# Kernel tuning notes

Measured on AMD Instinct MI355X. Metric: run time of the kernel, lower is better.

Reference implementation:

```python
import jax, jax.numpy as jnp
import numpy as np

T, B, F, H, P = 256, 512, 256, 512, 12  # seq len, batch, feature_dim, hidden_dim, p_interval


def setup_inputs() -> dict:
    key = jax.random.key(0)
    ks = jax.random.split(key, 9)
    s = 1.0 / np.sqrt(F + H)  # torch Linear default init scale
    def lin(k):
        kw, kb = jax.random.split(k)
        W = jax.random.uniform(kw, (F + H, H), jnp.float32, -s, s)
        b = jax.random.uniform(kb, (H,), jnp.float32, -s, s)
        return W, b
    Wf, bf = lin(ks[0])
    Wi, bi = lin(ks[1])
    Wo, bo = lin(ks[2])
    Wg, bg = lin(ks[3])
    x = jax.random.normal(ks[4], (T, B, F), jnp.float32)
    return {"x": x, "Wf": Wf, "bf": bf, "Wi": Wi, "bi": bi,
            "Wo": Wo, "bo": bo, "Wg": Wg, "bg": bg}


def _slstm(x, Wf, bf, Wi, bi, Wo, bo, Wg, bg):
    Tn, Bn, _ = x.shape
    h0 = jnp.zeros((P, Bn, H), x.dtype)
    # NOTE: original torch code reassigns c to a 2D [B,H] tensor after step 0,
    # so c[t % P] indexes a batch ROW (shape [H]) that broadcasts. At t=0 the
    # slice is all-zeros either way, so carrying a 2D c is exactly faithful.
    c0 = jnp.zeros((Bn, H), x.dtype)

    def step(carry, inp):
        h, c = carry
        x_t, t = inp
        idx = t % P
        xc = jnp.concatenate([x_t, h[idx]], axis=1)  # [B, F+H]
        f = jax.nn.softmax(xc @ Wf + bf, axis=1)
        i = jax.nn.softmax(xc @ Wi + bi, axis=1)
        o = jax.nn.softmax(xc @ Wo + bo, axis=1)
        g = jnp.tanh(xc @ Wg + bg)
        c_new = jnp.tanh(f * c[idx] + i * g)  # c[idx]: row [H], broadcasts over B
        h = h.at[idx].set(o * c_new)
        return (h, c_new), None

    (h, _), _ = jax.lax.scan(step, (h0, c0), (x, jnp.arange(Tn)))
    return h[(Tn - 1) % P]


def reference(x, Wf, bf, Wi, bi, Wo, bo, Wg, bg):
    return _slstm(x, Wf, bf, Wi, bi, Wo, bo, Wg, bg)
```

## Files before the change

### kernel.cpp

```cpp
#include <hip/hip_runtime.h>

typedef unsigned short u16;
typedef unsigned int   u32;

typedef __attribute__((ext_vector_type(8))) short bf16x8;
typedef __attribute__((ext_vector_type(16))) float f32x16;

__device__ __forceinline__ u16 f2bf(float v) {
    u32 u = __float_as_uint(v);
    u32 r = (u + 0x7fffu + ((u >> 16) & 1u)) >> 16;
    return (u16)r;
}
__device__ __forceinline__ float bf2f(u16 h) { return __uint_as_float(((u32)h) << 16); }

__device__ __forceinline__ float ftanh(float x) {
    float e = __expf(2.0f * x);
    return 1.0f - 2.0f * __builtin_amdgcn_rcpf(e + 1.0f);
}

__device__ __forceinline__ void gl2lds16(const void* g, void* l) {
    __builtin_amdgcn_global_load_lds(
        (const __attribute__((address_space(1))) void*)g,
        (__attribute__((address_space(3))) void*)l, 16, 0, 0);
}

__global__ void init_k(u16* __restrict__ hh, u16* __restrict__ hl, float* __restrict__ cb) {
    int i = blockIdx.x * 256 + threadIdx.x;
    hh[i] = 0; hl[i] = 0;
    if (i < 2 * 512) cb[i] = 0.0f;
}

__global__ void pack_w(const float* __restrict__ Wf, const float* __restrict__ bf_,
                       const float* __restrict__ Wi, const float* __restrict__ bi_,
                       const float* __restrict__ Wo, const float* __restrict__ bo_,
                       const float* __restrict__ Wg, const float* __restrict__ bg_,
                       u16* __restrict__ wth, u16* __restrict__ wtl, float* __restrict__ bias4) {
    int idx = blockIdx.x * 256 + threadIdx.x;
    int n = idx / 768, k = idx - n * 768;
    int gate = n >> 9, col = n & 511;
    const float* W = (gate == 0) ? Wf : (gate == 1) ? Wi : (gate == 2) ? Wo : Wg;
    float v = W[k * 512 + col];
    u16 h = f2bf(v);
    wth[idx] = h;
    wtl[idx] = f2bf(v - bf2f(h));
    if (k == 0) {
        const float* bb = (gate == 0) ? bf_ : (gate == 1) ? bi_ : (gate == 2) ? bo_ : bg_;
        bias4[n] = bb[col];
    }
}

__global__ void split_x(const float* __restrict__ src, u16* __restrict__ oh, u16* __restrict__ ol) {
    int i = blockIdx.x * 256 + threadIdx.x;
    float4 v = ((const float4*)src)[i];
    u16 hx = f2bf(v.x), hy = f2bf(v.y), hz = f2bf(v.z), hw = f2bf(v.w);
    u16 lx = f2bf(v.x - bf2f(hx)), ly = f2bf(v.y - bf2f(hy));
    u16 lz = f2bf(v.z - bf2f(hz)), lw = f2bf(v.w - bf2f(hw));
    uint2 hv; hv.x = (u32)hx | ((u32)hy << 16); hv.y = (u32)hz | ((u32)hw << 16);
    uint2 lv; lv.x = (u32)lx | ((u32)ly << 16); lv.y = (u32)lz | ((u32)lw << 16);
    ((uint2*)oh)[i] = hv;
    ((uint2*)ol)[i] = lv;
}

#define BK 32
__global__ __launch_bounds__(256, 3) void gemm_x3(
    const u16* __restrict__ xh, const u16* __restrict__ xl,
    const u16* __restrict__ hh, const u16* __restrict__ hl,
    const u16* __restrict__ wth, const u16* __restrict__ wtl,
    const float* __restrict__ bias4, float* __restrict__ lg) {
    __shared__ __align__(16) u16 Ah[128 * BK];
    __shared__ __align__(16) u16 Al[128 * BK];
    __shared__ __align__(16) u16 Bh[128 * BK];
    __shared__ __align__(16) u16 Bl[128 * BK];

    const int tid = threadIdx.x;
    const int wid = tid >> 6, lane = tid & 63;
    const int bm = blockIdx.x, bn = blockIdx.y;
    const int s = bm >> 2;
    const int b0 = (bm & 3) * 128;
    const int laneR = lane >> 2;
    const int laneC = (lane & 3) * 8;

    u16* lds = (wid == 0) ? Ah : (wid == 1) ? Al : (wid == 2) ? Bh : Bl;
    const u16* xp = (wid == 0) ? xh : xl;
    const u16* hp = (wid == 0) ? hh : hl;
    const u16* wp = (wid == 2) ? wth : wtl;
    const u16* xrow = xp + (size_t)(s * 512 + b0) * 256 + laneR * 256 + laneC;
    const u16* hrow = hp + (size_t)(s * 512 + b0) * 512 + laneR * 512 + laneC;
    const u16* wrow = wp + (size_t)(bn * 128) * 768 + laneR * 768 + laneC;

    const int wm = wid >> 1, wn = wid & 1;
    const int l32 = lane & 31, khalf = lane >> 5;

    f32x16 acc[2][2];
#pragma unroll
    for (int i = 0; i < 2; i++)
#pragma unroll
        for (int j = 0; j < 2; j++)
#pragma unroll
            for (int r = 0; r < 16; ++r) acc[i][j][r] = 0.f;

    for (int k0 = 0; k0 < 768; k0 += BK) {
        __syncthreads();
        if (wid < 2) {
            if (k0 < 256) {
                const u16* src = xrow + k0;
#pragma unroll
                for (int r = 0; r < 8; ++r) gl2lds16(src + r * 16 * 256, lds + r * 16 * BK);
            } else {
                const u16* src = hrow + (k0 - 256);
#pragma unroll
                for (int r = 0; r < 8; ++r) gl2lds16(src + r * 16 * 512, lds + r * 16 * BK);
            }
        } else {
            const u16* src = wrow + k0;
#pragma unroll
            for (int r = 0; r < 8; ++r) gl2lds16(src + r * 16 * 768, lds + r * 16 * BK);
        }
        __syncthreads();

        bf16x8 a_h[2][2], a_l[2][2], b_h[2][2], b_l[2][2];
#pragma unroll
        for (int t = 0; t < 2; ++t)
#pragma unroll
            for (int ks = 0; ks < 2; ++ks) {
                int ko = ks * 16 + khalf * 8;
                a_h[t][ks] = *(const bf16x8*)&Ah[(wm * 64 + t * 32 + l32) * BK + ko];
                a_l[t][ks] = *(const bf16x8*)&Al[(wm * 64 + t * 32 + l32) * BK + ko];
                b_h[t][ks] = *(const bf16x8*)&Bh[(wn * 64 + t * 32 + l32) * BK + ko];
                b_l[t][ks] = *(const bf16x8*)&Bl[(wn * 64 + t * 32 + l32) * BK + ko];
            }
#pragma unroll
        for (int ks = 0; ks < 2; ++ks)
#pragma unroll
            for (int i = 0; i < 2; ++i)
#pragma unroll
                for (int j = 0; j < 2; ++j) {
                    acc[i][j] = __builtin_amdgcn_mfma_f32_32x32x16_bf16(a_h[i][ks], b_h[j][ks], acc[i][j], 0, 0, 0);
                    acc[i][j] = __builtin_amdgcn_mfma_f32_32x32x16_bf16(a_h[i][ks], b_l[j][ks], acc[i][j], 0, 0, 0);
                    acc[i][j] = __builtin_amdgcn_mfma_f32_32x32x16_bf16(a_l[i][ks], b_h[j][ks], acc[i][j], 0, 0, 0);
                }
    }

#pragma unroll
    for (int j = 0; j < 2; ++j) {
        int n = bn * 128 + wn * 64 + j * 32 + l32;
        float bv = bias4[n];
#pragma unroll
        for (int i = 0; i < 2; ++i) {
            int rbase = wm * 64 + i * 32 + 4 * khalf;
#pragma unroll
            for (int r = 0; r < 16; ++r) {
                int row = rbase + (r & 3) + 8 * (r >> 2);
                __builtin_nontemporal_store(acc[i][j][r] + bv,
                    &lg[(size_t)(bm * 128 + row) * 2048 + n]);
            }
        }
    }
}

__device__ __forceinline__ void chain_step(const float* __restrict__ lg, int j, int lane, float r[8]) {
    int rowb = (j + 1) % 12;
    const float* base = lg + (size_t)(j * 512 + rowb) * 2048 + lane * 8;
    float f[8], iv[8], g[8];
#pragma unroll
    for (int u = 0; u < 8; ++u) { f[u] = base[u]; iv[u] = base[512 + u]; g[u] = base[1536 + u]; }
    float mf = -1e30f, mi = -1e30f;
#pragma unroll
    for (int u = 0; u < 8; ++u) { mf = fmaxf(mf, f[u]); mi = fmaxf(mi, iv[u]); }
#pragma unroll
    for (int o = 32; o; o >>= 1) { mf = fmaxf(mf, __shfl_xor(mf, o)); mi = fmaxf(mi, __shfl_xor(mi, o)); }
    float sf = 0.f, si = 0.f;
#pragma unroll
    for (int u = 0; u < 8; ++u) {
        f[u] = __expf(f[u] - mf); sf += f[u];
        iv[u] = __expf(iv[u] - mi); si += iv[u];
    }
#pragma unroll
    for (int o = 32; o; o >>= 1) { sf += __shfl_xor(sf, o); si += __shfl_xor(si, o); }
    float rf = __builtin_amdgcn_rcpf(sf), ri = __builtin_amdgcn_rcpf(si);
#pragma unroll
    for (int u = 0; u < 8; ++u) {
        float gg = ftanh(g[u]);
        r[u] = ftanh(f[u] * rf * r[u] + iv[u] * ri * gg);
    }
}

__global__ __launch_bounds__(256) void gates_k(
    const float* __restrict__ lg, float* __restrict__ cb,
    u16* __restrict__ hh, u16* __restrict__ hl,
    float* __restrict__ out, int t0, int S, int rd, int wr) {
    __shared__ float rsh[512];
    const int widx = threadIdx.x >> 6, lane = threadIdx.x & 63;
    const int s = (S - 1) - (blockIdx.x >> 7);
    const int b = (blockIdx.x & 127) * 4 + widx;
    const int t = t0 + s;

    if (widx == 0) {
        float r[8];
#pragma unroll
        for (int u = 0; u < 8; ++u) r[u] = cb[rd * 512 + lane * 8 + u];
        for (int j = 0; j < s; ++j) chain_step(lg, j, lane, r);
#pragma unroll
        for (int u = 0; u < 8; ++u) rsh[lane * 8 + u] = r[u];
        if ((int)blockIdx.x == 127 && t0 + S < 256) {
            chain_step(lg, S - 1, lane, r);
#pragma unroll
            for (int u = 0; u < 8; ++u) cb[wr * 512 + lane * 8 + u] = r[u];
        }
    }
    __syncthreads();

    const float* row = lg + (size_t)(s * 512 + b) * 2048 + lane * 8;
    float f[8], iv[8], ov[8], g[8];
#pragma unroll
    for (int u = 0; u < 8; ++u) {
        f[u] = row[u]; iv[u] = row[512 + u]; ov[u] = row[1024 + u]; g[u] = row[1536 + u];
    }
    float mf = -1e30f, mi = -1e30f, mo = -1e30f;
#pragma unroll
    for (int u = 0; u < 8; ++u) { mf = fmaxf(mf, f[u]); mi = fmaxf(mi, iv[u]); mo = fmaxf(mo, ov[u]); }
#pragma unroll
    for (int o = 32; o; o >>= 1) {
        mf = fmaxf(mf, __shfl_xor(mf, o));
        mi = fmaxf(mi, __shfl_xor(mi, o));
        mo = fmaxf(mo, __shfl_xor(mo, o));
    }
    float sf = 0.f, si = 0.f, so = 0.f;
#pragma unroll
    for (int u = 0; u < 8; ++u) {
        f[u] = __expf(f[u] - mf); sf += f[u];
        iv[u] = __expf(iv[u] - mi); si += iv[u];
        ov[u] = __expf(ov[u] - mo); so += ov[u];
    }
#pragma unroll
    for (int o = 32; o; o >>= 1) {
        sf += __shfl_xor(sf, o); si += __shfl_xor(si, o); so += __shfl_xor(so, o);
    }
    float rf = __builtin_amdgcn_rcpf(sf), ri = __builtin_amdgcn_rcpf(si), ro = __builtin_amdgcn_rcpf(so);
    float hout[8];
#pragma unroll
    for (int u = 0; u < 8; ++u) {
        float rr = rsh[lane * 8 + u];
        float gg = ftanh(g[u]);
        float cv = ftanh(f[u] * rf * rr + iv[u] * ri * gg);
        hout[u] = ov[u] * ro * cv;
    }
    u32 hhp[4], hlp[4];
#pragma unroll
    for (int u = 0; u < 4; ++u) {
        u16 h0 = f2bf(hout[2 * u]), h1 = f2bf(hout[2 * u + 1]);
        u16 l0 = f2bf(hout[2 * u] - bf2f(h0)), l1 = f2bf(hout[2 * u + 1] - bf2f(h1));
        hhp[u] = (u32)h0 | ((u32)h1 << 16);
        hlp[u] = (u32)l0 | ((u32)l1 << 16);
    }
    size_t hb = ((size_t)(s * 512 + b)) * 512 + lane * 8;
    *(uint4*)&hh[hb] = make_uint4(hhp[0], hhp[1], hhp[2], hhp[3]);
    *(uint4*)&hl[hb] = make_uint4(hlp[0], hlp[1], hlp[2], hlp[3]);
    if (t == 255) {
        float* op = out + (size_t)b * 512 + lane * 8;
#pragma unroll
        for (int u = 0; u < 8; ++u) op[u] = hout[u];
    }
}

extern "C" void kernel_launch(void* const* d_in, const int* in_sizes, int n_in,
                              void* d_out, int out_size, void* d_ws, size_t ws_size,
                              hipStream_t stream) {
    const float* x   = (const float*)d_in[0];
    const float* Wf  = (const float*)d_in[1];
    const float* bf_ = (const float*)d_in[2];
    const float* Wi  = (const float*)d_in[3];
    const float* bi_ = (const float*)d_in[4];
    const float* Wo  = (const float*)d_in[5];
    const float* bo_ = (const float*)d_in[6];
    const float* Wg  = (const float*)d_in[7];
    const float* bg_ = (const float*)d_in[8];
    float* out = (float*)d_out;

    char* p = (char*)d_ws;
    u16* xh  = (u16*)p; p += 134217728;
    u16* xl  = (u16*)p; p += 134217728;
    u16* wth = (u16*)p; p += 3145728;
    u16* wtl = (u16*)p; p += 3145728;
    u16* hh  = (u16*)p; p += 6291456;
    u16* hl  = (u16*)p; p += 6291456;
    float* bias4 = (float*)p; p += 8192;
    float* cb    = (float*)p; p += 4096;
    float* lg    = (float*)p; p += 50331648;

    init_k<<<12288, 256, 0, stream>>>(hh, hl, cb);
    pack_w<<<6144, 256, 0, stream>>>(Wf, bf_, Wi, bi_, Wo, bo_, Wg, bg_, wth, wtl, bias4);
    split_x<<<32768, 256, 0, stream>>>(x, xh, xl);

    for (int blk = 0; blk < 22; ++blk) {
        int t0 = blk * 12;
        int S = (256 - t0 >= 12) ? 12 : (256 - t0);
        gemm_x3<<<dim3(S * 4, 16), 256, 0, stream>>>(
            xh + (size_t)t0 * 512 * 256, xl + (size_t)t0 * 512 * 256,
            hh, hl, wth, wtl, bias4, lg);
        gates_k<<<S * 128, 256, 0, stream>>>(lg, cb, hh, hl, out, t0, S, blk & 1, (blk + 1) & 1);
    }
}
```

Baseline: 1.975 ms.

## Double-buffer activation tiles in LDS and stream weights directly from global

The activation (A) tiles in the split-bf16 GEMM now use a two-stage LDS buffer. The next K-slice is prefetched with global-to-LDS loads while the current one is consumed, so each iteration needs one barrier instead of two. The weight (B) tiles no longer go through LDS: each wave reads its bf16 high and low fragments straight from global memory into registers. This cuts LDS traffic and synchronization, but exposes global-load latency for the weights and makes both waves sharing a column slice fetch the same weight data redundantly.

```diff
diff --git a/kernel.cpp b/kernel.cpp
--- a/kernel.cpp
+++ b/kernel.cpp
@@ -67,10 +67,7 @@
     const u16* __restrict__ hh, const u16* __restrict__ hl,
     const u16* __restrict__ wth, const u16* __restrict__ wtl,
     const float* __restrict__ bias4, float* __restrict__ lg) {
-    __shared__ __align__(16) u16 Ah[128 * BK];
-    __shared__ __align__(16) u16 Al[128 * BK];
-    __shared__ __align__(16) u16 Bh[128 * BK];
-    __shared__ __align__(16) u16 Bl[128 * BK];
+    __shared__ __align__(16) u16 Abuf[2][2][128 * BK];
 
     const int tid = threadIdx.x;
     const int wid = tid >> 6, lane = tid & 63;
@@ -80,17 +77,18 @@
     const int laneR = lane >> 2;
     const int laneC = (lane & 3) * 8;
 
-    u16* lds = (wid == 0) ? Ah : (wid == 1) ? Al : (wid == 2) ? Bh : Bl;
     const u16* xp = (wid == 0) ? xh : xl;
     const u16* hp = (wid == 0) ? hh : hl;
-    const u16* wp = (wid == 2) ? wth : wtl;
     const u16* xrow = xp + (size_t)(s * 512 + b0) * 256 + laneR * 256 + laneC;
     const u16* hrow = hp + (size_t)(s * 512 + b0) * 512 + laneR * 512 + laneC;
-    const u16* wrow = wp + (size_t)(bn * 128) * 768 + laneR * 768 + laneC;
 
     const int wm = wid >> 1, wn = wid & 1;
     const int l32 = lane & 31, khalf = lane >> 5;
 
+    const size_t brow = (size_t)(bn * 128 + wn * 64 + l32) * 768 + khalf * 8;
+    const u16* bhp = wth + brow;
+    const u16* blp = wtl + brow;
+
     f32x16 acc[2][2];
 #pragma unroll
     for (int i = 0; i < 2; i++)
@@ -98,36 +96,49 @@
         for (int j = 0; j < 2; j++)
 #pragma unroll
             for (int r = 0; r < 16; ++r) acc[i][j][r] = 0.f;
+
+    if (wid < 2) {
+        u16* dst = Abuf[0][wid];
+#pragma unroll
+        for (int r = 0; r < 8; ++r) gl2lds16(xrow + r * 16 * 256, dst + r * 16 * BK);
+    }
 
     for (int k0 = 0; k0 < 768; k0 += BK) {
         __syncthreads();
-        if (wid < 2) {
-            if (k0 < 256) {
-                const u16* src = xrow + k0;
-#pragma unroll
-                for (int r = 0; r < 8; ++r) gl2lds16(src + r * 16 * 256, lds + r * 16 * BK);
+        const int cur = (k0 / BK) & 1;
+        if (wid < 2 && k0 + BK < 768) {
+            u16* dst = Abuf[cur ^ 1][wid];
+            int k1 = k0 + BK;
+            if (k1 < 256) {
+                const u16* src = xrow + k1;
+#pragma unroll
+                for (int r = 0; r < 8; ++r) gl2lds16(src + r * 16 * 256, dst + r * 16 * BK);
             } else {
-                const u16* src = hrow + (k0 - 256);
-#pragma unroll
-                for (int r = 0; r < 8; ++r) gl2lds16(src + r * 16 * 512, lds + r * 16 * BK);
+                const u16* src = hrow + (k1 - 256);
+#pragma unroll
+                for (int r = 0; r < 8; ++r) gl2lds16(src + r * 16 * 512, dst + r * 16 * BK);
             }
-        } else {
-            const u16* src = wrow + k0;
-#pragma unroll
-            for (int r = 0; r < 8; ++r) gl2lds16(src + r * 16 * 768, lds + r * 16 * BK);
         }
-        __syncthreads();
-
-        bf16x8 a_h[2][2], a_l[2][2], b_h[2][2], b_l[2][2];
+
+        bf16x8 b_h[2][2], b_l[2][2];
 #pragma unroll
         for (int t = 0; t < 2; ++t)
 #pragma unroll
             for (int ks = 0; ks < 2; ++ks) {
-                int ko = ks * 16 + khalf * 8;
-                a_h[t][ks] = *(const bf16x8*)&Ah[(wm * 64 + t * 32 + l32) * BK + ko];
-                a_l[t][ks] = *(const bf16x8*)&Al[(wm * 64 + t * 32 + l32) * BK + ko];
-                b_h[t][ks] = *(const bf16x8*)&Bh[(wn * 64 + t * 32 + l32) * BK + ko];
-                b_l[t][ks] = *(const bf16x8*)&Bl[(wn * 64 + t * 32 + l32) * BK + ko];
+                b_h[t][ks] = *(const bf16x8*)(bhp + (size_t)t * 32 * 768 + k0 + ks * 16);
+                b_l[t][ks] = *(const bf16x8*)(blp + (size_t)t * 32 * 768 + k0 + ks * 16);
+            }
+
+        const u16* Ah = Abuf[cur][0];
+        const u16* Al = Abuf[cur][1];
+        bf16x8 a_h[2][2], a_l[2][2];
+#pragma unroll
+        for (int t = 0; t < 2; ++t)
+#pragma unroll
+            for (int ks = 0; ks < 2; ++ks) {
+                int off = (wm * 64 + t * 32 + l32) * BK + ks * 16 + khalf * 8;
+                a_h[t][ks] = *(const bf16x8*)&Ah[off];
+                a_l[t][ks] = *(const bf16x8*)&Al[off];
             }
 #pragma unroll
         for (int ks = 0; ks < 2; ++ks)
```

Result: slower. 2.563 ms (+29.8%).

## Double-buffer A tiles in LDS, load B directly to registers, swizzle LDS

Applied to the files above, without the earlier changes.

The gemm_x3 main loop now double-buffers the activation (A) tiles in LDS, so the global-to-LDS copy for the next K slice overlaps the MFMAs on the current one. Weight (B) fragments no longer go through LDS. Each wave reads them straight from global memory into registers, one step ahead. An XOR swizzle on the LDS column offset is meant to reduce bank conflicts on the A fragment reads. The cost is more registers for two sets of B fragments, which may pressure the 3-blocks-per-SM launch bound, and B is now read redundantly from global by two waves.

```diff
diff --git a/kernel.cpp b/kernel.cpp
--- a/kernel.cpp
+++ b/kernel.cpp
@@ -67,10 +67,7 @@
     const u16* __restrict__ hh, const u16* __restrict__ hl,
     const u16* __restrict__ wth, const u16* __restrict__ wtl,
     const float* __restrict__ bias4, float* __restrict__ lg) {
-    __shared__ __align__(16) u16 Ah[128 * BK];
-    __shared__ __align__(16) u16 Al[128 * BK];
-    __shared__ __align__(16) u16 Bh[128 * BK];
-    __shared__ __align__(16) u16 Bl[128 * BK];
+    __shared__ __align__(16) u16 Abuf[2][2][128 * BK];
 
     const int tid = threadIdx.x;
     const int wid = tid >> 6, lane = tid & 63;
@@ -78,19 +75,20 @@
     const int s = bm >> 2;
     const int b0 = (bm & 3) * 128;
     const int laneR = lane >> 2;
-    const int laneC = (lane & 3) * 8;
-
-    u16* lds = (wid == 0) ? Ah : (wid == 1) ? Al : (wid == 2) ? Bh : Bl;
+    const int laneC = (((lane & 3) ^ (laneR & 3)) * 8);
+
     const u16* xp = (wid == 0) ? xh : xl;
     const u16* hp = (wid == 0) ? hh : hl;
-    const u16* wp = (wid == 2) ? wth : wtl;
     const u16* xrow = xp + (size_t)(s * 512 + b0) * 256 + laneR * 256 + laneC;
     const u16* hrow = hp + (size_t)(s * 512 + b0) * 512 + laneR * 512 + laneC;
-    const u16* wrow = wp + (size_t)(bn * 128) * 768 + laneR * 768 + laneC;
 
     const int wm = wid >> 1, wn = wid & 1;
     const int l32 = lane & 31, khalf = lane >> 5;
 
+    const size_t brow = (size_t)(bn * 128 + wn * 64 + l32) * 768 + khalf * 8;
+    const u16* bhp = wth + brow;
+    const u16* blp = wtl + brow;
+
     f32x16 acc[2][2];
 #pragma unroll
     for (int i = 0; i < 2; i++)
@@ -99,46 +97,73 @@
 #pragma unroll
             for (int r = 0; r < 16; ++r) acc[i][j][r] = 0.f;
 
-    for (int k0 = 0; k0 < 768; k0 += BK) {
+#define STAGE_A(buf, k1)                                                          \
+    do {                                                                          \
+        u16* dst = Abuf[buf][wid];                                                \
+        if ((k1) < 256) {                                                         \
+            const u16* src = xrow + (k1);                                         \
+            _Pragma("unroll")                                                     \
+            for (int r = 0; r < 8; ++r) gl2lds16(src + r * 16 * 256, dst + r * 16 * BK); \
+        } else {                                                                  \
+            const u16* src = hrow + ((k1) - 256);                                 \
+            _Pragma("unroll")                                                     \
+            for (int r = 0; r < 8; ++r) gl2lds16(src + r * 16 * 512, dst + r * 16 * BK); \
+        }                                                                         \
+    } while (0)
+
+#define LOAD_B(bh, bl, k1)                                                        \
+    do {                                                                          \
+        _Pragma("unroll")                                                         \
+        for (int t = 0; t < 2; ++t)                                               \
+            _Pragma("unroll")                                                     \
+            for (int ks = 0; ks < 2; ++ks) {                                      \
+                bh[t][ks] = *(const bf16x8*)(bhp + (size_t)t * 32 * 768 + (k1) + ks * 16); \
+                bl[t][ks] = *(const bf16x8*)(blp + (size_t)t * 32 * 768 + (k1) + ks * 16); \
+            }                                                                     \
+    } while (0)
+
+#define COMPUTE(cur, bh, bl)                                                      \
+    do {                                                                          \
+        const u16* Ah = Abuf[cur][0];                                             \
+        const u16* Al = Abuf[cur][1];                                             \
+        bf16x8 a_h[2][2], a_l[2][2];                                              \
+        _Pragma("unroll")                                                         \
+        for (int t = 0; t < 2; ++t)                                               \
+            _Pragma("unroll")                                                     \
+            for (int ks = 0; ks < 2; ++ks) {                                      \
+                int row = wm * 64 + t * 32 + l32;                                 \
+                int off = row * BK + (((2 * ks + khalf) ^ (l32 & 3)) * 8);        \
+                a_h[t][ks] = *(const bf16x8*)&Ah[off];                            \
+                a_l[t][ks] = *(const bf16x8*)&Al[off];                            \
+            }                                                                     \
+        _Pragma("unroll")                                                         \
+        for (int ks = 0; ks < 2; ++ks)                                            \
+            _Pragma("unroll")                                                     \
+            for (int i = 0; i < 2; ++i)                                           \
+                _Pragma("unroll")                                                 \
+                for (int j = 0; j < 2; ++j) {                                     \
+                    acc[i][j] = __builtin_amdgcn_mfma_f32_32x32x16_bf16(a_h[i][ks], bh[j][ks], acc[i][j], 0, 0, 0); \
+                    acc[i][j] = __builtin_amdgcn_mfma_f32_32x32x16_bf16(a_h[i][ks], bl[j][ks], acc[i][j], 0, 0, 0); \
+                    acc[i][j] = __builtin_amdgcn_mfma_f32_32x32x16_bf16(a_l[i][ks], bh[j][ks], acc[i][j], 0, 0, 0); \
+                }                                                                 \
+    } while (0)
+
+    bf16x8 bh0[2][2], bl0[2][2], bh1[2][2], bl1[2][2];
+
+    if (wid < 2) STAGE_A(0, 0);
+    LOAD_B(bh0, bl0, 0);
+
+#pragma unroll 1
+    for (int ko = 0; ko < 12; ++ko) {
+        const int k0 = ko * 64;
         __syncthreads();
-        if (wid < 2) {
-            if (k0 < 256) {
-                const u16* src = xrow + k0;
-#pragma unroll
-                for (int r = 0; r < 8; ++r) gl2lds16(src + r * 16 * 256, lds + r * 16 * BK);
-            } else {
-                const u16* src = hrow + (k0 - 256);
-#pragma unroll
-                for (int r = 0; r < 8; ++r) gl2lds16(src + r * 16 * 512, lds + r * 16 * BK);
-            }
-        } else {
-            const u16* src = wrow + k0;
-#pragma unroll
-            for (int r = 0; r < 8; ++r) gl2lds16(src + r * 16 * 768, lds + r * 16 * BK);
-        }
+        if (wid < 2) STAGE_A(1, k0 + BK);
+        LOAD_B(bh1, bl1, k0 + BK);
+        COMPUTE(0, bh0, bl0);
         __syncthreads();
-
-        bf16x8 a_h[2][2], a_l[2][2], b_h[2][2], b_l[2][2];
-#pragma unroll
-        for (int t = 0; t < 2; ++t)
-#pragma unroll
-            for (int ks = 0; ks < 2; ++ks) {
-                int ko = ks * 16 + khalf * 8;
-                a_h[t][ks] = *(const bf16x8*)&Ah[(wm * 64 + t * 32 + l32) * BK + ko];
-                a_l[t][ks] = *(const bf16x8*)&Al[(wm * 64 + t * 32 + l32) * BK + ko];
-                b_h[t][ks] = *(const bf16x8*)&Bh[(wn * 64 + t * 32 + l32) * BK + ko];
-                b_l[t][ks] = *(const bf16x8*)&Bl[(wn * 64 + t * 32 + l32) * BK + ko];
-            }
-#pragma unroll
-        for (int ks = 0; ks < 2; ++ks)
-#pragma unroll
-            for (int i = 0; i < 2; ++i)
-#pragma unroll
-                for (int j = 0; j < 2; ++j) {
-                    acc[i][j] = __builtin_amdgcn_mfma_f32_32x32x16_bf16(a_h[i][ks], b_h[j][ks], acc[i][j], 0, 0, 0);
-                    acc[i][j] = __builtin_amdgcn_mfma_f32_32x32x16_bf16(a_h[i][ks], b_l[j][ks], acc[i][j], 0, 0, 0);
-                    acc[i][j] = __builtin_amdgcn_mfma_f32_32x32x16_bf16(a_l[i][ks], b_h[j][ks], acc[i][j], 0, 0, 0);
-                }
+        if (wid < 2 && k0 + 2 * BK < 768) STAGE_A(0, k0 + 2 * BK);
+        if (k0 + 2 * BK < 768) LOAD_B(bh0, bl0, k0 + 2 * BK);
+        COMPUTE(1, bh1, bl1);
     }
 
 #pragma unroll
@@ -156,6 +181,9 @@
             }
         }
     }
+#undef STAGE_A
+#undef LOAD_B
+#undef COMPUTE
 }
 
 __device__ __forceinline__ void chain_step(const float* __restrict__ lg, int j, int lane, float r[8]) {
```

New measurement: 2.472 ms. 1.25x slower.
